# Kernel tuning notes

Measured on AMD Instinct MI355X. Metric: run time of the kernel, lower is better.

## Reference

```python
import jax, jax.numpy as jnp
import numpy as np

N, E = 20000, 320000
D_IN, H1, H2, H3, D_OUT = 2048, 512, 128, 32, 2
EPS = 1e-5


def layer_norm(x, g, b):
    mu = jnp.mean(x, axis=-1, keepdims=True)
    var = jnp.mean(jnp.square(x - mu), axis=-1, keepdims=True)
    return (x - mu) * jax.lax.rsqrt(var + EPS) * g + b


def gcn_conv(x, src, dst, n, W, b):
    # x' = D^{-1/2} A_hat D^{-1/2} (x W) + b  (self-loops already in src/dst)
    xw = x @ W
    deg = jax.ops.segment_sum(jnp.ones_like(src, dtype=x.dtype), dst, num_segments=n)
    dinv = jnp.where(deg > 0, jax.lax.rsqrt(jnp.maximum(deg, 1.0)), 0.0)
    norm = dinv[src] * dinv[dst]  # [E+N]
    msg = xw[src] * norm[:, None]
    return jax.ops.segment_sum(msg, dst, num_segments=n) + b


def gat_conv(x, src, dst, n, W, a_src, a_dst, b):
    # single-head GAT, concat=False; PyG defaults: LeakyReLU(0.2), softmax over dst
    xw = x @ W  # [N, H3]
    alpha = jax.nn.leaky_relu(xw[src] @ a_src + xw[dst] @ a_dst, 0.2)  # [E+N]
    amax = jax.ops.segment_max(alpha, dst, num_segments=n)
    e = jnp.exp(alpha - amax[dst])
    denom = jax.ops.segment_sum(e, dst, num_segments=n)
    coef = e / denom[dst]
    out = jax.ops.segment_sum(xw[src] * coef[:, None], dst, num_segments=n)
    return out + b


def setup_inputs() -> dict:
    key = jax.random.key(0)
    ks = jax.random.split(key, 24)
    x = jax.random.normal(ks[0], (N, D_IN), dtype=jnp.float32)
    edge_index = jax.random.randint(ks[1], (2, E), 0, N, dtype=jnp.int64)

    def glorot(k, shape):
        lim = float(np.sqrt(6.0 / (shape[0] + shape[1])))
        return jax.random.uniform(k, shape, jnp.float32, -lim, lim)

    return {
        "x": x, "edge_index": edge_index,
        "W1": glorot(ks[2], (D_IN, H1)), "b1": jnp.zeros((H1,), jnp.float32),
        "ln1_g": jnp.ones((H1,), jnp.float32), "ln1_b": jnp.zeros((H1,), jnp.float32),
        "W2": glorot(ks[3], (H1, H2)), "b2": jnp.zeros((H2,), jnp.float32),
        "ln2_g": jnp.ones((H2,), jnp.float32), "ln2_b": jnp.zeros((H2,), jnp.float32),
        "W3": glorot(ks[4], (H2, H3)), "b3": jnp.zeros((H3,), jnp.float32),
        "ln3_g": jnp.ones((H3,), jnp.float32), "ln3_b": jnp.zeros((H3,), jnp.float32),
        "Wg": glorot(ks[5], (H3, H3)),
        "att_src": jax.random.normal(ks[6], (H3,), jnp.float32) * 0.1,
        "att_dst": jax.random.normal(ks[7], (H3,), jnp.float32) * 0.1,
        "bg": jnp.zeros((H3,), jnp.float32),
        "fc_w": glorot(ks[8], (H3, D_OUT)), "fc_b": jnp.zeros((D_OUT,), jnp.float32),
    }


def reference(x, edge_index, W1, b1, ln1_g, ln1_b, W2, b2, ln2_g, ln2_b,
              W3, b3, ln3_g, ln3_b, Wg, att_src, att_dst, bg, fc_w, fc_b):
    n = x.shape[0]
    loops = jnp.arange(n, dtype=edge_index.dtype)
    src = jnp.concatenate([edge_index[0], loops])
    dst = jnp.concatenate([edge_index[1], loops])

    h = jax.nn.relu(layer_norm(gcn_conv(x, src, dst, n, W1, b1), ln1_g, ln1_b))
    h = jax.nn.relu(layer_norm(gcn_conv(h, src, dst, n, W2, b2), ln2_g, ln2_b))
    h = jax.nn.relu(layer_norm(gcn_conv(h, src, dst, n, W3, b3), ln3_g, ln3_b))
    h = jax.nn.relu(gat_conv(h, src, dst, n, Wg, att_src, att_dst, bg))
    pooled = jnp.mean(h, axis=0, keepdims=True)  # [1, H3]
    return pooled @ fc_w + fc_b  # [1, 2]
```

## Files before the change

kernel.cpp:

```cpp
#include <hip/hip_runtime.h>
#include <hip/hip_bf16.h>
#include <cstdint>
#include <cstddef>

#define N_NODES 20000
#define N_EDGES 320000
#define DIM_IN  2048
#define DIM_H1  512
#define DIM_H2  128
#define DIM_H3  32
#define NPART   64
static constexpr float LN_EPS = 1e-5f;

typedef __bf16 bf16x8 __attribute__((ext_vector_type(8)));
typedef __bf16 bf16x2 __attribute__((ext_vector_type(2)));
typedef float f32x4 __attribute__((ext_vector_type(4)));

__device__ __forceinline__ void glds16(const void* g, void* l) {
  __builtin_amdgcn_global_load_lds(
      (const __attribute__((address_space(1))) unsigned int*)g,
      (__attribute__((address_space(3))) unsigned int*)l, 16, 0, 0);
}

__global__ void detect_fmt_kernel(const void* eraw, int* flag) {
  const int2* p = (const int2*)eraw;
  int all0 = 1;
  for (int i = 0; i < 32; ++i) if (p[i].y != 0) all0 = 0;
  *flag = all0;
}

__global__ void convert_edges_kernel(const void* eraw, const int* __restrict__ flag,
                                     int* __restrict__ src, int* __restrict__ dst,
                                     int* __restrict__ cnt, int E) {
  const int is64 = *flag;
  for (int e = blockIdx.x * blockDim.x + threadIdx.x; e < E; e += gridDim.x * blockDim.x) {
    int s, d;
    if (is64) {
      const long long* p = (const long long*)eraw;
      s = (int)p[e];
      d = (int)p[(size_t)E + e];
    } else {
      const int* p = (const int*)eraw;
      s = p[e];
      d = p[(size_t)E + e];
    }
    src[e] = s;
    dst[e] = d;
    atomicAdd(&cnt[d], 1);
  }
}

__global__ __launch_bounds__(1024) void scan_kernel(const int* __restrict__ cnt,
                                                    int* __restrict__ rowptr,
                                                    int* __restrict__ cursor,
                                                    float* __restrict__ dinv, int n) {
  __shared__ int s[1024];
  const int t = threadIdx.x;
  const int chunk = (n + 1023) / 1024;
  const int beg = t * chunk;
  const int end = min(beg + chunk, n);
  int sum = 0;
  for (int i = beg; i < end; ++i) sum += cnt[i];
  s[t] = sum;
  __syncthreads();
  for (int d = 1; d < 1024; d <<= 1) {
    int v = (t >= d) ? s[t - d] : 0;
    __syncthreads();
    s[t] += v;
    __syncthreads();
  }
  int run = s[t] - sum;
  for (int i = beg; i < end; ++i) {
    rowptr[i] = run;
    cursor[i] = run;
    run += cnt[i];
    dinv[i] = rsqrtf((float)(cnt[i] + 1));
  }
  if (t == 1023) rowptr[n] = s[1023];
}

__global__ void scatter_kernel(const int* __restrict__ src, const int* __restrict__ dst,
                               int* __restrict__ cursor, int* __restrict__ csr_src, int E) {
  for (int e = blockIdx.x * blockDim.x + threadIdx.x; e < E; e += gridDim.x * blockDim.x) {
    int d = dst[e];
    int pos = atomicAdd(&cursor[d], 1);
    csr_src[pos] = src[e];
  }
}

__global__ __launch_bounds__(256) void transpose_cvt_kernel(const float* __restrict__ W,
                                                            __bf16* __restrict__ WT,
                                                            int K, int N) {
  __shared__ float t[32][33];
  const int kb = blockIdx.x * 32, nb = blockIdx.y * 32;
  const int tx = threadIdx.x & 31, ty = threadIdx.x >> 5;
  #pragma unroll
  for (int i = 0; i < 32; i += 8)
    t[ty + i][tx] = W[(size_t)(kb + ty + i) * N + nb + tx];
  __syncthreads();
  #pragma unroll
  for (int i = 0; i < 32; i += 8)
    WT[(size_t)(nb + ty + i) * K + kb + tx] = (__bf16)t[tx][ty + i];
}

template <int NCOL, typename AT, typename CT>
__global__ __launch_bounds__(256) void gemm_dbuf_kernel(
    const AT* __restrict__ A, const __bf16* __restrict__ BT,
    CT* __restrict__ C, int M, int N, int K) {
  const int Mtiles = (M + 127) >> 7;
  int mtile, cblk;
  if constexpr (NCOL == 1) {
    mtile = blockIdx.x;
    cblk = 0;
  } else {
    const int p = blockIdx.x;
    const int xcd = p & 7, slot = p >> 3;
    cblk = slot & (NCOL - 1);
    mtile = (slot / NCOL) * 8 + xcd;
    if (mtile >= Mtiles) return;
  }
  __shared__ __align__(16) AT     Asm[2][128 * 32];
  __shared__ __align__(16) __bf16 Bsm[2][128 * 32];
  const int tid = threadIdx.x;
  const int wave = tid >> 6;
  const int lane = tid & 63;
  const int row0 = mtile * 128;
  const int col0 = cblk * 128;
  const int wr = (wave >> 1) * 64;
  const int wc = (wave & 1) * 64;
  constexpr int NGLDS = (sizeof(AT) == 4) ? 6 : 4;

  f32x4 acc[4][4] = {};

  auto STAGE = [&](int buf, int k0) {
    if constexpr (sizeof(AT) == 4) {
      #pragma unroll
      for (int i = 0; i < 4; ++i) {
        const int rbase = wave * 32 + i * 8;
        int gr = row0 + rbase + (lane >> 3);
        if (gr >= M) gr = M - 1;
        const int ssrc = (lane & 7) ^ (lane >> 3);
        glds16((const float*)A + (size_t)gr * K + k0 + ssrc * 4, &Asm[buf][rbase * 32]);
      }
    } else {
      #pragma unroll
      for (int i = 0; i < 2; ++i) {
        const int rbase = wave * 32 + i * 16;
        int gr = row0 + rbase + (lane >> 2);
        if (gr >= M) gr = M - 1;
        const int ssrc = (lane & 3) ^ ((lane >> 3) & 3);
        glds16((const __bf16*)A + (size_t)gr * K + k0 + ssrc * 8, &Asm[buf][rbase * 32]);
      }
    }
    #pragma unroll
    for (int j = 0; j < 2; ++j) {
      const int rbase = wave * 32 + j * 16;
      const int gr = col0 + rbase + (lane >> 2);
      const int ssrc = (lane & 3) ^ ((lane >> 3) & 3);
      glds16(BT + (size_t)gr * K + k0 + ssrc * 8, &Bsm[buf][rbase * 32]);
    }
  };

  const int NT = K / 32;
  STAGE(0, 0);

  for (int t = 0; t < NT; ++t) {
    const int cur = t & 1;
    if (t + 1 < NT) {
      STAGE(cur ^ 1, (t + 1) * 32);
      asm volatile("s_waitcnt vmcnt(%0)" :: "i"(NGLDS) : "memory");
    } else {
      asm volatile("s_waitcnt vmcnt(0)" ::: "memory");
    }
    __builtin_amdgcn_s_barrier();
    __builtin_amdgcn_sched_barrier(0);

    const int q = lane >> 4;
    bf16x8 af[4], bfr[4];
    #pragma unroll
    for (int m = 0; m < 4; ++m) {
      const int row = wr + m * 16 + (lane & 15);
      if constexpr (sizeof(AT) == 4) {
        const int sw = row & 7;
        f32x4 lo = *(const f32x4*)&((const float*)&Asm[cur][0])[row * 32 + (((2 * q) ^ sw) * 4)];
        f32x4 hi = *(const f32x4*)&((const float*)&Asm[cur][0])[row * 32 + (((2 * q + 1) ^ sw) * 4)];
        bf16x8 o;
        o[0] = (__bf16)lo[0]; o[1] = (__bf16)lo[1]; o[2] = (__bf16)lo[2]; o[3] = (__bf16)lo[3];
        o[4] = (__bf16)hi[0]; o[5] = (__bf16)hi[1]; o[6] = (__bf16)hi[2]; o[7] = (__bf16)hi[3];
        af[m] = o;
      } else {
        const int sw = (row >> 1) & 3;
        af[m] = *(const bf16x8*)&((const __bf16*)&Asm[cur][0])[row * 32 + ((q ^ sw) * 8)];
      }
    }
    #pragma unroll
    for (int n = 0; n < 4; ++n) {
      const int row = wc + n * 16 + (lane & 15);
      const int sw = (row >> 1) & 3;
      bfr[n] = *(const bf16x8*)&Bsm[cur][row * 32 + ((q ^ sw) * 8)];
    }
    #pragma unroll
    for (int m = 0; m < 4; ++m)
      #pragma unroll
      for (int n = 0; n < 4; ++n)
        acc[m][n] = __builtin_amdgcn_mfma_f32_16x16x32_bf16(af[m], bfr[n], acc[m][n], 0, 0, 0);

    __builtin_amdgcn_sched_barrier(0);
    __builtin_amdgcn_s_barrier();
  }

  #pragma unroll
  for (int m = 0; m < 4; ++m) {
    const int r = row0 + wr + m * 16 + (lane >> 4) * 4;
    #pragma unroll
    for (int n = 0; n < 4; ++n) {
      const int c = col0 + wc + n * 16 + (lane & 15);
      #pragma unroll
      for (int j = 0; j < 4; ++j)
        if (r + j < M) C[(size_t)(r + j) * N + c] = (CT)acc[m][n][j];
    }
  }
}

template <int F, int TPB, typename OutT>
__global__ __launch_bounds__(TPB) void gcn_agg_ln_relu_kernel(
    const float* __restrict__ xw, const float* __restrict__ dinv,
    const int* __restrict__ rowptr, const int* __restrict__ csr_src,
    const float* __restrict__ bias, const float* __restrict__ gamma,
    const float* __restrict__ beta, OutT* __restrict__ h) {
  constexpr int NF = (F + TPB - 1) / TPB;
  const int i = blockIdx.x;
  const int tid = threadIdx.x;
  const float di = dinv[i];
  float acc[NF];
  #pragma unroll
  for (int q = 0; q < NF; ++q) {
    int f = tid + q * TPB;
    acc[q] = (f < F) ? di * xw[(size_t)i * F + f] : 0.f;
  }
  const int beg = rowptr[i], end = rowptr[i + 1];
  for (int j = beg; j < end; ++j) {
    int s = csr_src[j];
    float c = dinv[s];
    const float* row = xw + (size_t)s * F;
    #pragma unroll
    for (int q = 0; q < NF; ++q) {
      int f = tid + q * TPB;
      if (f < F) acc[q] += c * row[f];
    }
  }
  float sum = 0.f, sumsq = 0.f;
  #pragma unroll
  for (int q = 0; q < NF; ++q) {
    int f = tid + q * TPB;
    if (f < F) {
      float v = di * acc[q] + bias[f];
      acc[q] = v;
      sum += v;
      sumsq += v * v;
    }
  }
  #pragma unroll
  for (int m = 32; m >= 1; m >>= 1) {
    sum += __shfl_xor(sum, m);
    sumsq += __shfl_xor(sumsq, m);
  }
  constexpr int NW = TPB / 64;
  __shared__ float red[2][NW];
  const int wid = tid >> 6, lane = tid & 63;
  if (lane == 0) { red[0][wid] = sum; red[1][wid] = sumsq; }
  __syncthreads();
  if (tid == 0) {
    float a = 0.f, b2 = 0.f;
    for (int w = 0; w < NW; ++w) { a += red[0][w]; b2 += red[1][w]; }
    red[0][0] = a;
    red[1][0] = b2;
  }
  __syncthreads();
  const float mu = red[0][0] / F;
  const float var = red[1][0] / F - mu * mu;
  const float rstd = rsqrtf(var + LN_EPS);
  #pragma unroll
  for (int q = 0; q < NF; ++q) {
    int f = tid + q * TPB;
    if (f < F) h[(size_t)i * F + f] = (OutT)fmaxf(0.f, (acc[q] - mu) * rstd * gamma[f] + beta[f]);
  }
}

template <int F, int TPB, typename OutT>
__global__ __launch_bounds__(TPB) void gcn_agg_ln_relu_bf16_kernel(
    const __bf16* __restrict__ xw, const float* __restrict__ dinv,
    const int* __restrict__ rowptr, const int* __restrict__ csr_src,
    const float* __restrict__ bias, const float* __restrict__ gamma,
    const float* __restrict__ beta, OutT* __restrict__ h) {
  static_assert(F == 2 * TPB, "layout");
  const int i = blockIdx.x;
  const int tid = threadIdx.x;
  const int f0 = tid * 2;
  const float di = dinv[i];
  bf16x2 v = *(const bf16x2*)&xw[(size_t)i * F + f0];
  float a0 = di * (float)v[0];
  float a1 = di * (float)v[1];
  const int beg = rowptr[i], end = rowptr[i + 1];
  for (int j = beg; j < end; ++j) {
    int s = csr_src[j];
    float c = dinv[s];
    bf16x2 r = *(const bf16x2*)&xw[(size_t)s * F + f0];
    a0 += c * (float)r[0];
    a1 += c * (float)r[1];
  }
  a0 = di * a0 + bias[f0];
  a1 = di * a1 + bias[f0 + 1];
  float sum = a0 + a1;
  float sumsq = a0 * a0 + a1 * a1;
  #pragma unroll
  for (int m = 32; m >= 1; m >>= 1) {
    sum += __shfl_xor(sum, m);
    sumsq += __shfl_xor(sumsq, m);
  }
  constexpr int NW = TPB / 64;
  __shared__ float red[2][NW];
  const int wid = tid >> 6, lane = tid & 63;
  if (lane == 0) { red[0][wid] = sum; red[1][wid] = sumsq; }
  __syncthreads();
  if (tid == 0) {
    float a = 0.f, b2 = 0.f;
    for (int w = 0; w < NW; ++w) { a += red[0][w]; b2 += red[1][w]; }
    red[0][0] = a;
    red[1][0] = b2;
  }
  __syncthreads();
  const float mu = red[0][0] / F;
  const float var = red[1][0] / F - mu * mu;
  const float rstd = rsqrtf(var + LN_EPS);
  float o0 = fmaxf(0.f, (a0 - mu) * rstd * gamma[f0] + beta[f0]);
  float o1 = fmaxf(0.f, (a1 - mu) * rstd * gamma[f0 + 1] + beta[f0 + 1]);
  if constexpr (sizeof(OutT) == 2) {
    bf16x2 o; o[0] = (__bf16)o0; o[1] = (__bf16)o1;
    *(bf16x2*)&((__bf16*)h)[(size_t)i * F + f0] = o;
  } else {
    float2 o = make_float2(o0, o1);
    *(float2*)&((float*)h)[(size_t)i * F + f0] = o;
  }
}

template <int BM, int BN, int BK, int TM, int TN>
__global__ __launch_bounds__((BM / TM) * (BN / TN)) void sgemm_kernel(
    const float* __restrict__ A, const float* __restrict__ B, float* __restrict__ C,
    int M, int N, int K) {
  constexpr int THREADS = (BM / TM) * (BN / TN);
  __shared__ float As[BK][BM + 4];
  __shared__ float Bs[BK][BN];
  const int tid = threadIdx.x;
  const int tcol = tid % (BN / TN);
  const int trow = tid / (BN / TN);
  const int row0 = blockIdx.y * BM;
  const int col0 = blockIdx.x * BN;
  float acc[TM][TN] = {};
  for (int k0 = 0; k0 < K; k0 += BK) {
    constexpr int A4 = BM * BK / 4;
    #pragma unroll
    for (int i = tid; i < A4; i += THREADS) {
      int r = i / (BK / 4);
      int c4 = i % (BK / 4);
      int gr = row0 + r;
      float4 v = make_float4(0.f, 0.f, 0.f, 0.f);
      if (gr < M) v = *(const float4*)(A + (size_t)gr * K + k0 + c4 * 4);
      As[c4 * 4 + 0][r] = v.x;
      As[c4 * 4 + 1][r] = v.y;
      As[c4 * 4 + 2][r] = v.z;
      As[c4 * 4 + 3][r] = v.w;
    }
    constexpr int B4 = BK * BN / 4;
    #pragma unroll
    for (int i = tid; i < B4; i += THREADS) {
      int r = i / (BN / 4);
      int c4 = i % (BN / 4);
      float4 v = *(const float4*)(B + (size_t)(k0 + r) * N + col0 + c4 * 4);
      *(float4*)(&Bs[r][c4 * 4]) = v;
    }
    __syncthreads();
    #pragma unroll
    for (int kk = 0; kk < BK; ++kk) {
      float ra[TM], rb[TN];
      #pragma unroll
      for (int i = 0; i < TM; ++i) ra[i] = As[kk][trow * TM + i];
      #pragma unroll
      for (int j = 0; j < TN; ++j) rb[j] = Bs[kk][tcol * TN + j];
      #pragma unroll
      for (int i = 0; i < TM; ++i)
        #pragma unroll
        for (int j = 0; j < TN; ++j) acc[i][j] = fmaf(ra[i], rb[j], acc[i][j]);
    }
    __syncthreads();
  }
  #pragma unroll
  for (int i = 0; i < TM; ++i) {
    int gr = row0 + trow * TM + i;
    if (gr >= M) continue;
    #pragma unroll
    for (int j = 0; j < TN; ++j) {
      int gc = col0 + tcol * TN + j;
      if (gc < N) C[(size_t)gr * N + gc] = acc[i][j];
    }
  }
}

__global__ void gat_sdots_kernel(const float* __restrict__ xwg,
                                 const float* __restrict__ att_src,
                                 const float* __restrict__ att_dst,
                                 float* __restrict__ s_src, float* __restrict__ s_dst, int n) {
  int gid = blockIdx.x * blockDim.x + threadIdx.x;
  int node = gid >> 5;
  int l = threadIdx.x & 31;
  if (node >= n) return;
  float v = xwg[(size_t)node * 32 + l];
  float vs = v * att_src[l];
  float vd = v * att_dst[l];
  #pragma unroll
  for (int m = 16; m >= 1; m >>= 1) {
    vs += __shfl_xor(vs, m);
    vd += __shfl_xor(vd, m);
  }
  if (l == 0) { s_src[node] = vs; s_dst[node] = vd; }
}

__device__ __forceinline__ float leaky02(float x) { return x > 0.f ? x : 0.2f * x; }

__global__ __launch_bounds__(64) void gat_agg_kernel(
    const float* __restrict__ xwg, const float* __restrict__ s_src,
    const float* __restrict__ s_dst, const int* __restrict__ rowptr,
    const int* __restrict__ csr_src, const float* __restrict__ bg,
    float* __restrict__ pooled_part) {
  const int i = blockIdx.x;
  const int lane = threadIdx.x;
  const int f = lane & 31;
  const int half = lane >> 5;
  const float sd = s_dst[i];
  float m, den, acc;
  if (half == 0) {
    m = leaky02(s_src[i] + sd);
    den = 1.f;
    acc = xwg[(size_t)i * 32 + f];
  } else {
    m = -3.0e38f;
    den = 0.f;
    acc = 0.f;
  }
  const int beg = rowptr[i], end = rowptr[i + 1];
  for (int j = beg + half; j < end; j += 2) {
    int s = csr_src[j];
    float a = leaky02(s_src[s] + sd);
    float mn = fmaxf(m, a);
    float sc = __expf(m - mn);
    float ea = __expf(a - mn);
    acc = acc * sc + ea * xwg[(size_t)s * 32 + f];
    den = den * sc + ea;
    m = mn;
  }
  float m_o = __shfl_xor(m, 32);
  float den_o = __shfl_xor(den, 32);
  float acc_o = __shfl_xor(acc, 32);
  float mn = fmaxf(m, m_o);
  float sc = __expf(m - mn);
  float so = __expf(m_o - mn);
  float den_t = den * sc + den_o * so;
  float acc_t = acc * sc + acc_o * so;
  float out = fmaxf(acc_t / den_t + bg[f], 0.f);
  if (lane < 32) atomicAdd(&pooled_part[(size_t)(i & (NPART - 1)) * 32 + f], out);
}

__global__ __launch_bounds__(64) void final_fc_kernel(const float* __restrict__ pooled_part,
                                                      const float* __restrict__ fc_w,
                                                      const float* __restrict__ fc_b,
                                                      float* __restrict__ out, float invN) {
  const int lane = threadIdx.x;
  const int f = lane & 31, half = lane >> 5;
  float p = 0.f;
  #pragma unroll
  for (int b = 0; b < NPART / 2; ++b)
    p += pooled_part[(size_t)(half * (NPART / 2) + b) * 32 + f];
  p += __shfl_xor(p, 32);
  p *= invN;
  #pragma unroll
  for (int c = 0; c < 2; ++c) {
    float v = (lane < 32) ? p * fc_w[f * 2 + c] : 0.f;
    #pragma unroll
    for (int m = 16; m >= 1; m >>= 1) v += __shfl_xor(v, m);
    if (lane == 0) out[c] = v + fc_b[c];
  }
}

extern "C" void kernel_launch(void* const* d_in, const int* in_sizes, int n_in,
                              void* d_out, int out_size, void* d_ws, size_t ws_size,
                              hipStream_t stream) {
  const float* x       = (const float*)d_in[0];
  const void*  edges   = d_in[1];
  const float* W1      = (const float*)d_in[2];
  const float* b1      = (const float*)d_in[3];
  const float* ln1_g   = (const float*)d_in[4];
  const float* ln1_b   = (const float*)d_in[5];
  const float* W2      = (const float*)d_in[6];
  const float* b2      = (const float*)d_in[7];
  const float* ln2_g   = (const float*)d_in[8];
  const float* ln2_b   = (const float*)d_in[9];
  const float* W3      = (const float*)d_in[10];
  const float* b3      = (const float*)d_in[11];
  const float* ln3_g   = (const float*)d_in[12];
  const float* ln3_b   = (const float*)d_in[13];
  const float* Wg      = (const float*)d_in[14];
  const float* att_src = (const float*)d_in[15];
  const float* att_dst = (const float*)d_in[16];
  const float* bg      = (const float*)d_in[17];
  const float* fc_w    = (const float*)d_in[18];
  const float* fc_b    = (const float*)d_in[19];
  float* out = (float*)d_out;

  const int N = N_NODES, E = N_EDGES;

  char* ws = (char*)d_ws;
  size_t off = 0;
  auto alloc = [&](size_t bytes) {
    size_t o = off;
    off = (off + bytes + 255) & ~(size_t)255;
    return o;
  };
  size_t o_bufA   = alloc((size_t)N * DIM_H1 * 4);
  size_t o_bufB   = alloc((size_t)N * DIM_H1 * 4);
  size_t o_w1t    = alloc((size_t)DIM_IN * DIM_H1 * 2);
  size_t o_w2t    = alloc((size_t)DIM_H1 * DIM_H2 * 2);
  size_t o_src    = alloc((size_t)E * 4);
  size_t o_dst    = alloc((size_t)E * 4);
  size_t o_csr    = alloc((size_t)E * 4);
  size_t o_cnt    = alloc((size_t)N * 4);
  size_t o_rowptr = alloc((size_t)(N + 1) * 4);
  size_t o_cursor = alloc((size_t)N * 4);
  size_t o_dinv   = alloc((size_t)N * 4);
  size_t o_ssrc   = alloc((size_t)N * 4);
  size_t o_sdst   = alloc((size_t)N * 4);
  size_t o_pooled = alloc((size_t)NPART * 32 * 4);
  size_t o_flag   = alloc(4);

  float* bufA   = (float*)(ws + o_bufA);
  float* bufB   = (float*)(ws + o_bufB);
  __bf16* W1T   = (__bf16*)(ws + o_w1t);
  __bf16* W2T   = (__bf16*)(ws + o_w2t);
  int*   srcI   = (int*)(ws + o_src);
  int*   dstI   = (int*)(ws + o_dst);
  int*   csr    = (int*)(ws + o_csr);
  int*   cnt    = (int*)(ws + o_cnt);
  int*   rowptr = (int*)(ws + o_rowptr);
  int*   cursor = (int*)(ws + o_cursor);
  float* dinv   = (float*)(ws + o_dinv);
  float* ssrc   = (float*)(ws + o_ssrc);
  float* sdst   = (float*)(ws + o_sdst);
  float* pooled = (float*)(ws + o_pooled);
  int*   flag   = (int*)(ws + o_flag);

  hipMemsetAsync(cnt, 0, (size_t)N * 4, stream);
  hipMemsetAsync(pooled, 0, (size_t)NPART * 32 * 4, stream);

  const int EB = (E + 255) / 256;

  detect_fmt_kernel<<<1, 1, 0, stream>>>(edges, flag);
  convert_edges_kernel<<<EB, 256, 0, stream>>>(edges, flag, srcI, dstI, cnt, E);
  scan_kernel<<<1, 1024, 0, stream>>>(cnt, rowptr, cursor, dinv, N);
  scatter_kernel<<<EB, 256, 0, stream>>>(srcI, dstI, cursor, csr, E);

  transpose_cvt_kernel<<<dim3(DIM_IN / 32, DIM_H1 / 32), 256, 0, stream>>>(W1, W1T, DIM_IN, DIM_H1);
  transpose_cvt_kernel<<<dim3(DIM_H1 / 32, DIM_H2 / 32), 256, 0, stream>>>(W2, W2T, DIM_H1, DIM_H2);

  const int MB128 = (N + 127) / 128;

  gemm_dbuf_kernel<4, float, __bf16>
      <<<((MB128 + 7) / 8) * 8 * 4, 256, 0, stream>>>(x, W1T, (__bf16*)bufA, N, DIM_H1, DIM_IN);
  gcn_agg_ln_relu_bf16_kernel<DIM_H1, 256, __bf16>
      <<<N, 256, 0, stream>>>((const __bf16*)bufA, dinv, rowptr, csr, b1, ln1_g, ln1_b, (__bf16*)bufB);

  gemm_dbuf_kernel<1, __bf16, __bf16>
      <<<MB128, 256, 0, stream>>>((const __bf16*)bufB, W2T, (__bf16*)bufA, N, DIM_H2, DIM_H1);
  gcn_agg_ln_relu_bf16_kernel<DIM_H2, 64, float>
      <<<N, 64, 0, stream>>>((const __bf16*)bufA, dinv, rowptr, csr, b2, ln2_g, ln2_b, bufB);

  sgemm_kernel<128, 32, 16, 8, 2>
      <<<dim3(1, MB128), 256, 0, stream>>>(bufB, W3, bufA, N, DIM_H3, DIM_H2);
  gcn_agg_ln_relu_kernel<DIM_H3, 64, float>
      <<<N, 64, 0, stream>>>(bufA, dinv, rowptr, csr, b3, ln3_g, ln3_b, bufB);

  sgemm_kernel<128, 32, 16, 8, 2>
      <<<dim3(1, MB128), 256, 0, stream>>>(bufB, Wg, bufA, N, DIM_H3, DIM_H3);
  gat_sdots_kernel<<<(N * 32 + 255) / 256, 256, 0, stream>>>(bufA, att_src, att_dst, ssrc, sdst, N);
  gat_agg_kernel<<<N, 64, 0, stream>>>(bufA, ssrc, sdst, rowptr, csr, bg, pooled);

  final_fc_kernel<<<1, 64, 0, stream>>>(pooled, fc_w, fc_b, out, 1.f / (float)N);
}
```

Baseline: 356.5 us.

## Shrink first GEMM M-tile to 96, unroll GCN gather, widen GAT aggregation

Templates the bf16 MFMA GEMM on the M-tile height and runs the first layer's 20000x2048x512 GEMM with 96-row tiles. This gives more blocks, for better CU fill and tail balance, at the cost of less A/B reuse per block. Separately, it unrolls the bf16 GCN neighbour-gather loop by four with two accumulator pairs to raise memory-level parallelism. It also widens the GAT aggregation to 128 threads with four edge groups merged via a shuffle and shared memory, which adds a block barrier.

```diff
diff --git a/kernel.cpp b/kernel.cpp
--- a/kernel.cpp
+++ b/kernel.cpp
@@ -103,11 +103,13 @@
     WT[(size_t)(nb + ty + i) * K + kb + tx] = (__bf16)t[tx][ty + i];
 }
 
-template <int NCOL, typename AT, typename CT>
+template <int BM, int NCOL, typename AT, typename CT>
 __global__ __launch_bounds__(256) void gemm_dbuf_kernel(
     const AT* __restrict__ A, const __bf16* __restrict__ BT,
     CT* __restrict__ C, int M, int N, int K) {
-  const int Mtiles = (M + 127) >> 7;
+  constexpr int MFR = BM / 32;
+  static_assert(sizeof(AT) == 2 ? (BM % 64 == 0) : (BM % 32 == 0), "staging");
+  const int Mtiles = (M + BM - 1) / BM;
   int mtile, cblk;
   if constexpr (NCOL == 1) {
     mtile = blockIdx.x;
@@ -119,24 +121,24 @@
     mtile = (slot / NCOL) * 8 + xcd;
     if (mtile >= Mtiles) return;
   }
-  __shared__ __align__(16) AT     Asm[2][128 * 32];
+  __shared__ __align__(16) AT     Asm[2][BM * 32];
   __shared__ __align__(16) __bf16 Bsm[2][128 * 32];
   const int tid = threadIdx.x;
   const int wave = tid >> 6;
   const int lane = tid & 63;
-  const int row0 = mtile * 128;
+  const int row0 = mtile * BM;
   const int col0 = cblk * 128;
-  const int wr = (wave >> 1) * 64;
+  const int wr = (wave >> 1) * (BM / 2);
   const int wc = (wave & 1) * 64;
-  constexpr int NGLDS = (sizeof(AT) == 4) ? 6 : 4;
-
-  f32x4 acc[4][4] = {};
+  constexpr int NGLDS = (sizeof(AT) == 4 ? BM / 32 : BM / 64) + 2;
+
+  f32x4 acc[MFR][4] = {};
 
   auto STAGE = [&](int buf, int k0) {
     if constexpr (sizeof(AT) == 4) {
       #pragma unroll
-      for (int i = 0; i < 4; ++i) {
-        const int rbase = wave * 32 + i * 8;
+      for (int i = 0; i < BM / 32; ++i) {
+        const int rbase = wave * (BM / 4) + i * 8;
         int gr = row0 + rbase + (lane >> 3);
         if (gr >= M) gr = M - 1;
         const int ssrc = (lane & 7) ^ (lane >> 3);
@@ -144,8 +146,8 @@
       }
     } else {
       #pragma unroll
-      for (int i = 0; i < 2; ++i) {
-        const int rbase = wave * 32 + i * 16;
+      for (int i = 0; i < BM / 64; ++i) {
+        const int rbase = wave * (BM / 4) + i * 16;
         int gr = row0 + rbase + (lane >> 2);
         if (gr >= M) gr = M - 1;
         const int ssrc = (lane & 3) ^ ((lane >> 3) & 3);
@@ -176,9 +178,9 @@
     __builtin_amdgcn_sched_barrier(0);
 
     const int q = lane >> 4;
-    bf16x8 af[4], bfr[4];
-    #pragma unroll
-    for (int m = 0; m < 4; ++m) {
+    bf16x8 af[MFR], bfr[4];
+    #pragma unroll
+    for (int m = 0; m < MFR; ++m) {
       const int row = wr + m * 16 + (lane & 15);
       if constexpr (sizeof(AT) == 4) {
         const int sw = row & 7;
@@ -200,7 +202,7 @@
       bfr[n] = *(const bf16x8*)&Bsm[cur][row * 32 + ((q ^ sw) * 8)];
     }
     #pragma unroll
-    for (int m = 0; m < 4; ++m)
+    for (int m = 0; m < MFR; ++m)
       #pragma unroll
       for (int n = 0; n < 4; ++n)
         acc[m][n] = __builtin_amdgcn_mfma_f32_16x16x32_bf16(af[m], bfr[n], acc[m][n], 0, 0, 0);
@@ -210,7 +212,7 @@
   }
 
   #pragma unroll
-  for (int m = 0; m < 4; ++m) {
+  for (int m = 0; m < MFR; ++m) {
     const int r = row0 + wr + m * 16 + (lane >> 4) * 4;
     #pragma unroll
     for (int n = 0; n < 4; ++n) {
@@ -301,14 +303,30 @@
   bf16x2 v = *(const bf16x2*)&xw[(size_t)i * F + f0];
   float a0 = di * (float)v[0];
   float a1 = di * (float)v[1];
+  float b0 = 0.f, b1 = 0.f;
   const int beg = rowptr[i], end = rowptr[i + 1];
-  for (int j = beg; j < end; ++j) {
+  int j = beg;
+  for (; j + 3 < end; j += 4) {
+    int s0 = csr_src[j], s1 = csr_src[j + 1], s2 = csr_src[j + 2], s3 = csr_src[j + 3];
+    float c0 = dinv[s0], c1 = dinv[s1], c2 = dinv[s2], c3 = dinv[s3];
+    bf16x2 r0 = *(const bf16x2*)&xw[(size_t)s0 * F + f0];
+    bf16x2 r1 = *(const bf16x2*)&xw[(size_t)s1 * F + f0];
+    bf16x2 r2 = *(const bf16x2*)&xw[(size_t)s2 * F + f0];
+    bf16x2 r3 = *(const bf16x2*)&xw[(size_t)s3 * F + f0];
+    a0 += c0 * (float)r0[0]; a1 += c0 * (float)r0[1];
+    b0 += c1 * (float)r1[0]; b1 += c1 * (float)r1[1];
+    a0 += c2 * (float)r2[0]; a1 += c2 * (float)r2[1];
+    b0 += c3 * (float)r3[0]; b1 += c3 * (float)r3[1];
+  }
+  for (; j < end; ++j) {
     int s = csr_src[j];
     float c = dinv[s];
     bf16x2 r = *(const bf16x2*)&xw[(size_t)s * F + f0];
     a0 += c * (float)r[0];
     a1 += c * (float)r[1];
   }
+  a0 += b0;
+  a1 += b1;
   a0 = di * a0 + bias[f0];
   a1 = di * a1 + bias[f0 + 1];
   float sum = a0 + a1;
@@ -427,18 +445,18 @@
 
 __device__ __forceinline__ float leaky02(float x) { return x > 0.f ? x : 0.2f * x; }
 
-__global__ __launch_bounds__(64) void gat_agg_kernel(
+__global__ __launch_bounds__(128) void gat_agg_kernel(
     const float* __restrict__ xwg, const float* __restrict__ s_src,
     const float* __restrict__ s_dst, const int* __restrict__ rowptr,
     const int* __restrict__ csr_src, const float* __restrict__ bg,
     float* __restrict__ pooled_part) {
   const int i = blockIdx.x;
-  const int lane = threadIdx.x;
-  const int f = lane & 31;
-  const int half = lane >> 5;
+  const int t = threadIdx.x;
+  const int f = t & 31;
+  const int grp = t >> 5;
   const float sd = s_dst[i];
   float m, den, acc;
-  if (half == 0) {
+  if (grp == 0) {
     m = leaky02(s_src[i] + sd);
     den = 1.f;
     acc = xwg[(size_t)i * 32 + f];
@@ -448,7 +466,7 @@
     acc = 0.f;
   }
   const int beg = rowptr[i], end = rowptr[i + 1];
-  for (int j = beg + half; j < end; j += 2) {
+  for (int j = beg + grp; j < end; j += 4) {
     int s = csr_src[j];
     float a = leaky02(s_src[s] + sd);
     float mn = fmaxf(m, a);
@@ -458,16 +476,30 @@
     den = den * sc + ea;
     m = mn;
   }
-  float m_o = __shfl_xor(m, 32);
-  float den_o = __shfl_xor(den, 32);
-  float acc_o = __shfl_xor(acc, 32);
-  float mn = fmaxf(m, m_o);
-  float sc = __expf(m - mn);
-  float so = __expf(m_o - mn);
-  float den_t = den * sc + den_o * so;
-  float acc_t = acc * sc + acc_o * so;
-  float out = fmaxf(acc_t / den_t + bg[f], 0.f);
-  if (lane < 32) atomicAdd(&pooled_part[(size_t)(i & (NPART - 1)) * 32 + f], out);
+  {
+    float m_o = __shfl_xor(m, 32);
+    float den_o = __shfl_xor(den, 32);
+    float acc_o = __shfl_xor(acc, 32);
+    float mn = fmaxf(m, m_o);
+    float sc = __expf(m - mn);
+    float so = __expf(m_o - mn);
+    den = den * sc + den_o * so;
+    acc = acc * sc + acc_o * so;
+    m = mn;
+  }
+  __shared__ float smem[3][32];
+  if (t >= 64 && t < 96) { smem[0][f] = m; smem[1][f] = den; smem[2][f] = acc; }
+  __syncthreads();
+  if (t < 32) {
+    float m_o = smem[0][f], den_o = smem[1][f], acc_o = smem[2][f];
+    float mn = fmaxf(m, m_o);
+    float sc = __expf(m - mn);
+    float so = __expf(m_o - mn);
+    float den_t = den * sc + den_o * so;
+    float acc_t = acc * sc + acc_o * so;
+    float out = fmaxf(acc_t / den_t + bg[f], 0.f);
+    atomicAdd(&pooled_part[(size_t)(i & (NPART - 1)) * 32 + f], out);
+  }
 }
 
 __global__ __launch_bounds__(64) void final_fc_kernel(const float* __restrict__ pooled_part,
@@ -571,13 +603,14 @@
   transpose_cvt_kernel<<<dim3(DIM_H1 / 32, DIM_H2 / 32), 256, 0, stream>>>(W2, W2T, DIM_H1, DIM_H2);
 
   const int MB128 = (N + 127) / 128;
-
-  gemm_dbuf_kernel<4, float, __bf16>
-      <<<((MB128 + 7) / 8) * 8 * 4, 256, 0, stream>>>(x, W1T, (__bf16*)bufA, N, DIM_H1, DIM_IN);
+  const int MB96  = (N + 95) / 96;
+
+  gemm_dbuf_kernel<96, 4, float, __bf16>
+      <<<((MB96 + 7) / 8) * 8 * 4, 256, 0, stream>>>(x, W1T, (__bf16*)bufA, N, DIM_H1, DIM_IN);
   gcn_agg_ln_relu_bf16_kernel<DIM_H1, 256, __bf16>
       <<<N, 256, 0, stream>>>((const __bf16*)bufA, dinv, rowptr, csr, b1, ln1_g, ln1_b, (__bf16*)bufB);
 
-  gemm_dbuf_kernel<1, __bf16, __bf16>
+  gemm_dbuf_kernel<128, 1, __bf16, __bf16>
       <<<MB128, 256, 0, stream>>>((const __bf16*)bufB, W2T, (__bf16*)bufA, N, DIM_H2, DIM_H1);
   gcn_agg_ln_relu_bf16_kernel<DIM_H2, 64, float>
       <<<N, 64, 0, stream>>>((const __bf16*)bufA, dinv, rowptr, csr, b2, ln2_g, ln2_b, bufB);
@@ -590,7 +623,7 @@
   sgemm_kernel<128, 32, 16, 8, 2>
       <<<dim3(1, MB128), 256, 0, stream>>>(bufB, Wg, bufA, N, DIM_H3, DIM_H3);
   gat_sdots_kernel<<<(N * 32 + 255) / 256, 256, 0, stream>>>(bufA, att_src, att_dst, ssrc, sdst, N);
-  gat_agg_kernel<<<N, 64, 0, stream>>>(bufA, ssrc, sdst, rowptr, csr, bg, pooled);
+  gat_agg_kernel<<<N, 128, 0, stream>>>(bufA, ssrc, sdst, rowptr, csr, bg, pooled);
 
   final_fc_kernel<<<1, 64, 0, stream>>>(pooled, fc_w, fc_b, out, 1.f / (float)N);
 }
```

Result: faster. 323.2 us (-9.3%).
